# Performance work log

Measured on AMD Instinct MI355X. Metric: run time of the kernel, lower is better.

Reference implementation:

```python
import jax, jax.numpy as jnp
import numpy as np

B, S, D = 2, 2048, 1024
H, A = 16, 64  # num_heads, attention_dim


def setup_inputs() -> dict:
    key = jax.random.key(0)
    ks = jax.random.split(key, 9)
    sd = D ** -0.5
    so = (H * A) ** -0.5
    return {
        "x": jax.random.normal(ks[0], (B, S, D), dtype=jnp.float32),
        "Wq": jax.random.normal(ks[1], (D, H * A), dtype=jnp.float32) * sd,
        "bq": jnp.zeros((H * A,), dtype=jnp.float32),
        "Wk": jax.random.normal(ks[2], (D, H * A), dtype=jnp.float32) * sd,
        "bk": jnp.zeros((H * A,), dtype=jnp.float32),
        "Wv": jax.random.normal(ks[3], (D, H * A), dtype=jnp.float32) * sd,
        "bv": jnp.zeros((H * A,), dtype=jnp.float32),
        "Wo": jax.random.normal(ks[4], (H * A, D), dtype=jnp.float32) * so,
        "bo": jnp.zeros((D,), dtype=jnp.float32),
    }


def reference(x, Wq, bq, Wk, bk, Wv, bv, Wo, bo):
    b, s, _ = x.shape
    # project and split heads: [b, s, H, A]
    q = (x @ Wq + bq).reshape(b, s, H, A)
    k = (x @ Wk + bk).reshape(b, s, H, A)
    v = (x @ Wv + bv).reshape(b, s, H, A)
    # scores [b, H, s, s]
    scores = jnp.einsum("bqhd,bkhd->bhqk", q, k) / jnp.sqrt(jnp.float32(A))
    weights = jax.nn.softmax(scores, axis=-1)
    attended = jnp.einsum("bhqk,bkhd->bqhd", weights, v).reshape(b, s, H * A)
    return attended @ Wo + bo
```

## Files before the change

### kernel.cpp

```cpp
#include <hip/hip_runtime.h>
#include <hip/hip_bf16.h>

typedef __attribute__((ext_vector_type(8))) short bf16x8;
typedef __attribute__((ext_vector_type(4))) float f32x4;

#define LOG2E 1.44269504088896f

extern "C" __device__ float __ocml_native_exp2_f32(float);

__device__ __forceinline__ unsigned short f2bf(float f) {
    union { float f; unsigned int u; } v; v.f = f;
    unsigned int r = v.u + 0x7FFF + ((v.u >> 16) & 1);
    return (unsigned short)(r >> 16);
}

__device__ __forceinline__ unsigned int pk_bf16(float lo, float hi) {
    unsigned int r;
    asm("v_cvt_pk_bf16_f32 %0, %1, %2" : "=v"(r) : "v"(lo), "v"(hi));
    return r;
}

typedef __attribute__((address_space(3))) unsigned int lds_uint;
typedef __attribute__((address_space(1))) const unsigned int glob_uint;
__device__ __forceinline__ void gl2lds16(const void* g, void* l) {
    __builtin_amdgcn_global_load_lds((glob_uint*)g, (lds_uint*)l, 16, 0, 0);
}

__global__ __launch_bounds__(256) void cvt_bf16(const float* __restrict__ in,
                                                unsigned int* __restrict__ out, int n4) {
    int i = blockIdx.x * 256 + threadIdx.x;
    if (i >= n4) return;
    float4 v = ((const float4*)in)[i];
    uint2 o;
    o.x = pk_bf16(v.x, v.y);
    o.y = pk_bf16(v.z, v.w);
    ((uint2*)out)[i] = o;
}

__global__ __launch_bounds__(256) void transpose4_bf16(
    const float* __restrict__ w0, const float* __restrict__ w1,
    const float* __restrict__ w2, const float* __restrict__ w3,
    unsigned short* __restrict__ o0, unsigned short* __restrict__ o1,
    unsigned short* __restrict__ o2, unsigned short* __restrict__ o3) {
    const int z = blockIdx.z;
    const float* in = (z == 0) ? w0 : (z == 1) ? w1 : (z == 2) ? w2 : w3;
    unsigned short* out = (z == 0) ? o0 : (z == 1) ? o1 : (z == 2) ? o2 : o3;
    __shared__ float t[32][33];
    int tx = threadIdx.x & 31, ty = threadIdx.x >> 5;
    int r0 = blockIdx.y * 32, c0 = blockIdx.x * 32;
    for (int i = 0; i < 32; i += 8)
        t[ty + i][tx] = in[(size_t)(r0 + ty + i) * 1024 + c0 + tx];
    __syncthreads();
    for (int i = 0; i < 32; i += 8)
        out[(size_t)(c0 + ty + i) * 1024 + r0 + tx] = f2bf(t[tx][ty + i]);
}

__device__ __forceinline__ void gemm_core(const short* __restrict__ A,
                                          const short* __restrict__ BT,
                                          int K, int bm0, int bn0,
                                          short* sm, f32x4 acc[4][4]) {
    const int tid = threadIdx.x;
    const int lane = tid & 63;
    const int w = tid >> 6;
    const int wr0 = (w >> 1) * 64;
    const int wc0 = (w & 1) * 64;
    const int l15 = lane & 15, quad = lane >> 4;
    const int sr = lane >> 2;
    const int slog = (lane & 3) ^ (sr & 3) ^ (sr >> 2);

#pragma unroll
    for (int i = 0; i < 4; i++)
#pragma unroll
        for (int j = 0; j < 4; j++) acc[i][j] = (f32x4)0.f;

    const short* sp[4];
    int sdo[4];
#pragma unroll
    for (int i = 0; i < 4; i++) {
        int c = w * 4 + i;
        sp[i] = (c < 8) ? A + (size_t)(bm0 + c * 16 + sr) * K + slog * 8
                        : BT + (size_t)(bn0 + (c - 8) * 16 + sr) * K + slog * 8;
        sdo[i] = c * 512;
    }
    auto stage = [&](int buf) {
        short* bb = sm + buf * 8192;
#pragma unroll
        for (int i = 0; i < 4; i++) {
            gl2lds16(sp[i], bb + sdo[i]);
            sp[i] += 32;
        }
    };
    const int ph = (quad ^ (l15 & 3) ^ (l15 >> 2)) * 8;
    auto compute = [&](int buf) {
        const short* Ab = sm + buf * 8192;
        const short* Bb = Ab + 4096;
        bf16x8 af[4], bfr[4];
#pragma unroll
        for (int im = 0; im < 4; im++)
            af[im] = *(const bf16x8*)&Ab[(wr0 + im * 16 + l15) * 32 + ph];
#pragma unroll
        for (int in = 0; in < 4; in++)
            bfr[in] = *(const bf16x8*)&Bb[(wc0 + in * 16 + l15) * 32 + ph];
        __builtin_amdgcn_s_setprio(1);
#pragma unroll
        for (int im = 0; im < 4; im++)
#pragma unroll
            for (int in = 0; in < 4; in++)
                acc[im][in] = __builtin_amdgcn_mfma_f32_16x16x32_bf16(af[im], bfr[in], acc[im][in], 0, 0, 0);
        __builtin_amdgcn_s_setprio(0);
    };

    stage(0); stage(1);
    asm volatile("s_waitcnt vmcnt(4)" ::: "memory");
    __builtin_amdgcn_s_barrier();
    asm volatile("" ::: "memory");

    const int nt = K >> 5;
    int bs = 2, bc = 0;
    for (int t = 0; t < nt - 2; ++t) {
        stage(bs); bs = (bs == 2) ? 0 : bs + 1;
        compute(bc); bc = (bc == 2) ? 0 : bc + 1;
        asm volatile("s_waitcnt vmcnt(4)" ::: "memory");
        __builtin_amdgcn_s_barrier();
        asm volatile("" ::: "memory");
    }
    compute(bc); bc = (bc == 2) ? 0 : bc + 1;
    asm volatile("s_waitcnt vmcnt(0)" ::: "memory");
    __builtin_amdgcn_s_barrier();
    asm volatile("" ::: "memory");
    compute(bc);
}

__global__ __launch_bounds__(256) void gemm_qkv(
    const short* __restrict__ xb,
    const short* __restrict__ wqT, const short* __restrict__ wkT, const short* __restrict__ wvT,
    const float* __restrict__ bq, const float* __restrict__ bk, const float* __restrict__ bv,
    unsigned short* __restrict__ qb, unsigned short* __restrict__ kb, unsigned short* __restrict__ vTb) {
    __shared__ short sm[24576];
    const int z = blockIdx.z;
    const short* Amat = (z == 2) ? wvT : xb;
    const short* Bmat = (z == 0) ? wqT : (z == 1) ? wkT : xb;
    const float* bias = (z == 0) ? bq : (z == 1) ? bk : bv;
    const float scl = (z == 0) ? 0.125f * LOG2E : 1.f;
    const int bm0 = (z == 2) ? blockIdx.y * 128 : blockIdx.x * 128;
    const int bn0 = (z == 2) ? blockIdx.x * 128 : blockIdx.y * 128;
    f32x4 acc[4][4];
    gemm_core(Amat, Bmat, 1024, bm0, bn0, sm, acc);
    const int lane = threadIdx.x & 63, w = threadIdx.x >> 6;
    const int wr0 = (w >> 1) * 64, wc0 = (w & 1) * 64, l15 = lane & 15, quad = lane >> 4;
    if (z == 2) {
        for (int im = 0; im < 4; im++)
            for (int in = 0; in < 4; in++)
                for (int r = 0; r < 4; r++) {
                    int rowa = bm0 + wr0 + im * 16 + quad * 4 + r;
                    int colg = bn0 + wc0 + in * 16 + l15;
                    unsigned short ov = f2bf(acc[im][in][r] + bias[rowa]);
                    int b = colg >> 11, s = colg & 2047;
                    vTb[(size_t)b * 2097152 + (size_t)rowa * 2048 + s] = ov;
                }
    } else {
        for (int im = 0; im < 4; im++)
            for (int in = 0; in < 4; in++)
                for (int r = 0; r < 4; r++) {
                    int rowg = bm0 + wr0 + im * 16 + quad * 4 + r;
                    int colg = bn0 + wc0 + in * 16 + l15;
                    unsigned short ov = f2bf((acc[im][in][r] + bias[colg]) * scl);
                    int b = rowg >> 11, s = rowg & 2047;
                    int h = colg >> 6, a = colg & 63;
                    int bh = b * 16 + h;
                    if (z == 0) qb[((size_t)bh * 2048 + s) * 64 + a] = ov;
                    else        kb[((size_t)bh * 2048 + s) * 64 + a] = ov;
                }
    }
}

__global__ __launch_bounds__(256) void gemm_out(
    const short* __restrict__ att, const short* __restrict__ woT,
    const float* __restrict__ bo, float* __restrict__ out) {
    __shared__ short sm[24576];
    const int bm0 = blockIdx.x * 128, bn0 = blockIdx.y * 128;
    f32x4 acc[4][4];
    gemm_core(att, woT, 1024, bm0, bn0, sm, acc);
    const int lane = threadIdx.x & 63, w = threadIdx.x >> 6;
    const int wr0 = (w >> 1) * 64, wc0 = (w & 1) * 64, l15 = lane & 15, quad = lane >> 4;
    for (int im = 0; im < 4; im++)
        for (int in = 0; in < 4; in++)
            for (int r = 0; r < 4; r++) {
                int rowg = bm0 + wr0 + im * 16 + quad * 4 + r;
                int colg = bn0 + wc0 + in * 16 + l15;
                out[(size_t)rowg * 1024 + colg] = acc[im][in][r] + bo[colg];
            }
}

__global__ __launch_bounds__(512, 4) void flash_attn(
    const unsigned short* __restrict__ qb, const unsigned short* __restrict__ kb,
    const unsigned short* __restrict__ vTb, unsigned short* __restrict__ att) {
    __shared__ short Qs[8192];
    __shared__ short Ks[4][4096];
    __shared__ short Vs[4][4096];
    const int tid = threadIdx.x, lane = tid & 63, w = tid >> 6;
    const int l15 = lane & 15, quad = lane >> 4;
    const int q0 = blockIdx.x * 128;
    const int bh = blockIdx.y;
    const size_t qkbase = (size_t)bh * 2048 * 64;
    const size_t vbase = (size_t)bh * 64 * 2048;
    const int sr = lane >> 3;
    const int slog = (lane & 7) ^ sr;
    const int l7 = l15 & 7;

    const unsigned short* sgp;
    int sgstep, sg2;
    short* sgb;
    if (w < 4) {
        sgp = kb + qkbase + (size_t)(w * 16 + sr) * 64 + slog * 8;
        sgstep = 4096; sg2 = 512;
        sgb = &Ks[0][0] + w * 1024;
    } else {
        sgp = vTb + vbase + (size_t)((w - 4) * 16 + sr) * 2048 + slog * 8;
        sgstep = 64; sg2 = 16384;
        sgb = &Vs[0][0] + (w - 4) * 1024;
    }
    auto stage_tile = [&](int buf) {
        short* sd = sgb + buf * 4096;
        gl2lds16(sgp, sd);
        gl2lds16(sgp + sg2, sd + 512);
        sgp += sgstep;
    };

    for (int i = 0; i < 2; i++) {
        int c = w * 2 + i;
        gl2lds16(qb + qkbase + (size_t)(q0 + c * 8 + sr) * 64 + slog * 8, Qs + c * 512);
    }
    stage_tile(0); stage_tile(1); stage_tile(2);
    asm volatile("s_waitcnt vmcnt(4)" ::: "memory");
    __builtin_amdgcn_s_barrier();
    asm volatile("" ::: "memory");

    const int wq0 = w * 16;
    const int c0 = (quad ^ l7) * 8, c1 = c0 ^ 32;
    const int fb = l15 * 64;
    bf16x8 aq0 = *(const bf16x8*)&Qs[(wq0 + l15) * 64 + c0];
    bf16x8 aq1 = *(const bf16x8*)&Qs[(wq0 + l15) * 64 + c1];

    f32x4 o[4];
    for (int dt = 0; dt < 4; dt++) o[dt] = (f32x4)0.f;
    f32x4 ls = (f32x4)0.f;

    auto attn_step = [&](int buf) {
        const short* Kb = &Ks[0][0] + buf * 4096;
        const short* Vb = &Vs[0][0] + buf * 4096;
        f32x4 sc[4];
        __builtin_amdgcn_s_setprio(1);
#pragma unroll
        for (int t = 0; t < 4; t++) {
            bf16x8 ak = *(const bf16x8*)(Kb + fb + c0 + t * 1024);
            sc[t] = __builtin_amdgcn_mfma_f32_16x16x32_bf16(ak, aq0, (f32x4)0.f, 0, 0, 0);
        }
#pragma unroll
        for (int t = 0; t < 4; t++) {
            bf16x8 ak = *(const bf16x8*)(Kb + fb + c1 + t * 1024);
            sc[t] = __builtin_amdgcn_mfma_f32_16x16x32_bf16(ak, aq1, sc[t], 0, 0, 0);
        }
        __builtin_amdgcn_s_setprio(0);
#pragma unroll
        for (int t = 0; t < 4; t++) {
#pragma unroll
            for (int r = 0; r < 4; r++) sc[t][r] = __ocml_native_exp2_f32(sc[t][r]);
            ls += sc[t];
        }
        bf16x8 bp[2];
#pragma unroll
        for (int t2 = 0; t2 < 2; t2++) {
            unsigned pa = pk_bf16(sc[2 * t2][0], sc[2 * t2][1]);
            unsigned pb = pk_bf16(sc[2 * t2][2], sc[2 * t2][3]);
            unsigned pc = pk_bf16(sc[2 * t2 + 1][0], sc[2 * t2 + 1][1]);
            unsigned pd = pk_bf16(sc[2 * t2 + 1][2], sc[2 * t2 + 1][3]);
            asm("v_permlane32_swap_b32 %0, %1" : "+v"(pa), "+v"(pc));
            asm("v_permlane32_swap_b32 %0, %1" : "+v"(pb), "+v"(pd));
            asm("v_permlane16_swap_b32 %0, %1" : "+v"(pa), "+v"(pc));
            asm("v_permlane16_swap_b32 %0, %1" : "+v"(pb), "+v"(pd));
            union { unsigned u[4]; bf16x8 v; } cvt;
            cvt.u[0] = pa; cvt.u[1] = pb; cvt.u[2] = pc; cvt.u[3] = pd;
            bp[t2] = cvt.v;
        }
        __builtin_amdgcn_s_setprio(1);
#pragma unroll
        for (int t2 = 0; t2 < 2; t2++) {
            const int cc = t2 ? c1 : c0;
#pragma unroll
            for (int dt = 0; dt < 4; dt++) {
                bf16x8 av = *(const bf16x8*)(Vb + fb + cc + dt * 1024);
                o[dt] = __builtin_amdgcn_mfma_f32_16x16x32_bf16(av, bp[t2], o[dt], 0, 0, 0);
            }
        }
        __builtin_amdgcn_s_setprio(0);
    };

    for (int t = 0; t < 29; t++) {
        stage_tile((t + 3) & 3);
        attn_step(t & 3);
        asm volatile("s_waitcnt vmcnt(4)" ::: "memory");
        __builtin_amdgcn_s_barrier();
        asm volatile("" ::: "memory");
    }
    attn_step(1);
    asm volatile("s_waitcnt vmcnt(2)" ::: "memory");
    __builtin_amdgcn_s_barrier();
    asm volatile("" ::: "memory");
    attn_step(2);
    asm volatile("s_waitcnt vmcnt(0)" ::: "memory");
    __builtin_amdgcn_s_barrier();
    asm volatile("" ::: "memory");
    attn_step(3);

    const int b = bh >> 4, h = bh & 15;
    float l = (ls[0] + ls[1]) + (ls[2] + ls[3]);
    l += __shfl_xor(l, 16);
    l += __shfl_xor(l, 32);
    float inv = 1.f / l;
    int s = q0 + wq0 + l15;
    for (int dt = 0; dt < 4; dt++) {
        uint2 pk;
        pk.x = pk_bf16(o[dt][0] * inv, o[dt][1] * inv);
        pk.y = pk_bf16(o[dt][2] * inv, o[dt][3] * inv);
        int col = h * 64 + dt * 16 + quad * 4;
        *(uint2*)&att[((size_t)b * 2048 + s) * 1024 + col] = pk;
    }
}

extern "C" void kernel_launch(void* const* d_in, const int* in_sizes, int n_in,
                              void* d_out, int out_size, void* d_ws, size_t ws_size,
                              hipStream_t stream) {
    const float* x  = (const float*)d_in[0];
    const float* Wq = (const float*)d_in[1];
    const float* bq = (const float*)d_in[2];
    const float* Wk = (const float*)d_in[3];
    const float* bk = (const float*)d_in[4];
    const float* Wv = (const float*)d_in[5];
    const float* bv = (const float*)d_in[6];
    const float* Wo = (const float*)d_in[7];
    const float* bo = (const float*)d_in[8];
    float* out = (float*)d_out;

    short* ws  = (short*)d_ws;
    short* xb  = ws;
    short* wqT = ws + 4 * 1024 * 1024;
    short* wkT = wqT + 1024 * 1024;
    short* wvT = wkT + 1024 * 1024;
    short* woT = wvT + 1024 * 1024;
    short* qb  = woT + 1024 * 1024;
    short* kb  = qb + 4 * 1024 * 1024;
    short* vTb = kb + 4 * 1024 * 1024;
    short* att = vTb + 4 * 1024 * 1024;

    cvt_bf16<<<4096, 256, 0, stream>>>(x, (unsigned int*)xb, 1024 * 1024);
    transpose4_bf16<<<dim3(32, 32, 4), 256, 0, stream>>>(
        Wq, Wk, Wv, Wo,
        (unsigned short*)wqT, (unsigned short*)wkT,
        (unsigned short*)wvT, (unsigned short*)woT);
    gemm_qkv<<<dim3(32, 8, 3), 256, 0, stream>>>(xb, wqT, wkT, wvT, bq, bk, bv,
                                                 (unsigned short*)qb, (unsigned short*)kb,
                                                 (unsigned short*)vTb);
    flash_attn<<<dim3(16, 32), 512, 0, stream>>>((const unsigned short*)qb,
                                                 (const unsigned short*)kb,
                                                 (const unsigned short*)vTb,
                                                 (unsigned short*)att);
    gemm_out<<<dim3(32, 8), 256, 0, stream>>>(att, woT, bo, out);
}
```

Baseline: 182.3 us.

## Halve flash-attention block to 4 waves, each wave processing 32 query rows

The flash attention kernel now runs 256 threads per block instead of 512. Each wave handles two 16-row query tiles and reuses every K and V fragment it loads from LDS for both tiles, which halves LDS reads per MFMA. Each wave also stages twice as many K/V chunks per tile, so the vmcnt waits are doubled to match. In exchange there is more register pressure from the doubled accumulators, fewer waves per block to hide latency, and an occupancy hint lowered to 2.

```diff
diff --git a/kernel.cpp b/kernel.cpp
--- a/kernel.cpp
+++ b/kernel.cpp
@@ -192,7 +192,7 @@
             }
 }
 
-__global__ __launch_bounds__(512, 4) void flash_attn(
+__global__ __launch_bounds__(256, 2) void flash_attn(
     const unsigned short* __restrict__ qb, const unsigned short* __restrict__ kb,
     const unsigned short* __restrict__ vTb, unsigned short* __restrict__ att) {
     __shared__ short Qs[8192];
@@ -209,66 +209,58 @@
     const int l7 = l15 & 7;
 
     const unsigned short* sgp;
-    int sgstep, sg2;
+    int sgstep, sgr;
     short* sgb;
-    if (w < 4) {
-        sgp = kb + qkbase + (size_t)(w * 16 + sr) * 64 + slog * 8;
-        sgstep = 4096; sg2 = 512;
-        sgb = &Ks[0][0] + w * 1024;
+    if (w < 2) {
+        sgp = kb + qkbase + (size_t)(w * 32 + sr) * 64 + slog * 8;
+        sgstep = 4096;
+        sgr = 512;
+        sgb = &Ks[0][0] + w * 2048;
     } else {
-        sgp = vTb + vbase + (size_t)((w - 4) * 16 + sr) * 2048 + slog * 8;
-        sgstep = 64; sg2 = 16384;
-        sgb = &Vs[0][0] + (w - 4) * 1024;
+        sgp = vTb + vbase + (size_t)((w - 2) * 32 + sr) * 2048 + slog * 8;
+        sgstep = 64;
+        sgr = 16384;
+        sgb = &Vs[0][0] + (w - 2) * 2048;
     }
     auto stage_tile = [&](int buf) {
         short* sd = sgb + buf * 4096;
         gl2lds16(sgp, sd);
-        gl2lds16(sgp + sg2, sd + 512);
+        gl2lds16(sgp + sgr, sd + 512);
+        gl2lds16(sgp + 2 * sgr, sd + 1024);
+        gl2lds16(sgp + 3 * sgr, sd + 1536);
         sgp += sgstep;
     };
 
-    for (int i = 0; i < 2; i++) {
-        int c = w * 2 + i;
+#pragma unroll
+    for (int i = 0; i < 4; i++) {
+        int c = w * 4 + i;
         gl2lds16(qb + qkbase + (size_t)(q0 + c * 8 + sr) * 64 + slog * 8, Qs + c * 512);
     }
     stage_tile(0); stage_tile(1); stage_tile(2);
-    asm volatile("s_waitcnt vmcnt(4)" ::: "memory");
-    __builtin_amdgcn_s_barrier();
-    asm volatile("" ::: "memory");
-
-    const int wq0 = w * 16;
+    asm volatile("s_waitcnt vmcnt(8)" ::: "memory");
+    __builtin_amdgcn_s_barrier();
+    asm volatile("" ::: "memory");
+
+    const int wq0 = w * 32;
     const int c0 = (quad ^ l7) * 8, c1 = c0 ^ 32;
     const int fb = l15 * 64;
-    bf16x8 aq0 = *(const bf16x8*)&Qs[(wq0 + l15) * 64 + c0];
-    bf16x8 aq1 = *(const bf16x8*)&Qs[(wq0 + l15) * 64 + c1];
-
-    f32x4 o[4];
-    for (int dt = 0; dt < 4; dt++) o[dt] = (f32x4)0.f;
-    f32x4 ls = (f32x4)0.f;
-
-    auto attn_step = [&](int buf) {
-        const short* Kb = &Ks[0][0] + buf * 4096;
-        const short* Vb = &Vs[0][0] + buf * 4096;
-        f32x4 sc[4];
-        __builtin_amdgcn_s_setprio(1);
+    bf16x8 aq00 = *(const bf16x8*)&Qs[(wq0 + l15) * 64 + c0];
+    bf16x8 aq01 = *(const bf16x8*)&Qs[(wq0 + l15) * 64 + c1];
+    bf16x8 aq10 = *(const bf16x8*)&Qs[(wq0 + 16 + l15) * 64 + c0];
+    bf16x8 aq11 = *(const bf16x8*)&Qs[(wq0 + 16 + l15) * 64 + c1];
+
+    f32x4 o0[4], o1[4];
+#pragma unroll
+    for (int dt = 0; dt < 4; dt++) { o0[dt] = (f32x4)0.f; o1[dt] = (f32x4)0.f; }
+    f32x4 ls0 = (f32x4)0.f, ls1 = (f32x4)0.f;
+
+    auto smax = [&](f32x4 (&sc)[4], f32x4& lsr, bf16x8 (&bp)[2]) {
 #pragma unroll
         for (int t = 0; t < 4; t++) {
-            bf16x8 ak = *(const bf16x8*)(Kb + fb + c0 + t * 1024);
-            sc[t] = __builtin_amdgcn_mfma_f32_16x16x32_bf16(ak, aq0, (f32x4)0.f, 0, 0, 0);
-        }
-#pragma unroll
-        for (int t = 0; t < 4; t++) {
-            bf16x8 ak = *(const bf16x8*)(Kb + fb + c1 + t * 1024);
-            sc[t] = __builtin_amdgcn_mfma_f32_16x16x32_bf16(ak, aq1, sc[t], 0, 0, 0);
-        }
-        __builtin_amdgcn_s_setprio(0);
-#pragma unroll
-        for (int t = 0; t < 4; t++) {
 #pragma unroll
             for (int r = 0; r < 4; r++) sc[t][r] = __ocml_native_exp2_f32(sc[t][r]);
-            ls += sc[t];
-        }
-        bf16x8 bp[2];
+            lsr += sc[t];
+        }
 #pragma unroll
         for (int t2 = 0; t2 < 2; t2++) {
             unsigned pa = pk_bf16(sc[2 * t2][0], sc[2 * t2][1]);
@@ -283,6 +275,29 @@
             cvt.u[0] = pa; cvt.u[1] = pb; cvt.u[2] = pc; cvt.u[3] = pd;
             bp[t2] = cvt.v;
         }
+    };
+
+    auto attn_step = [&](int buf) {
+        const short* Kb = &Ks[0][0] + buf * 4096;
+        const short* Vb = &Vs[0][0] + buf * 4096;
+        f32x4 sc0[4], sc1[4];
+        __builtin_amdgcn_s_setprio(1);
+#pragma unroll
+        for (int t = 0; t < 4; t++) {
+            bf16x8 ak = *(const bf16x8*)(Kb + fb + c0 + t * 1024);
+            sc0[t] = __builtin_amdgcn_mfma_f32_16x16x32_bf16(ak, aq00, (f32x4)0.f, 0, 0, 0);
+            sc1[t] = __builtin_amdgcn_mfma_f32_16x16x32_bf16(ak, aq10, (f32x4)0.f, 0, 0, 0);
+        }
+#pragma unroll
+        for (int t = 0; t < 4; t++) {
+            bf16x8 ak = *(const bf16x8*)(Kb + fb + c1 + t * 1024);
+            sc0[t] = __builtin_amdgcn_mfma_f32_16x16x32_bf16(ak, aq01, sc0[t], 0, 0, 0);
+            sc1[t] = __builtin_amdgcn_mfma_f32_16x16x32_bf16(ak, aq11, sc1[t], 0, 0, 0);
+        }
+        __builtin_amdgcn_s_setprio(0);
+        bf16x8 bp0[2], bp1[2];
+        smax(sc0, ls0, bp0);
+        smax(sc1, ls1, bp1);
         __builtin_amdgcn_s_setprio(1);
 #pragma unroll
         for (int t2 = 0; t2 < 2; t2++) {
@@ -290,7 +305,8 @@
 #pragma unroll
             for (int dt = 0; dt < 4; dt++) {
                 bf16x8 av = *(const bf16x8*)(Vb + fb + cc + dt * 1024);
-                o[dt] = __builtin_amdgcn_mfma_f32_16x16x32_bf16(av, bp[t2], o[dt], 0, 0, 0);
+                o0[dt] = __builtin_amdgcn_mfma_f32_16x16x32_bf16(av, bp0[t2], o0[dt], 0, 0, 0);
+                o1[dt] = __builtin_amdgcn_mfma_f32_16x16x32_bf16(av, bp1[t2], o1[dt], 0, 0, 0);
             }
         }
         __builtin_amdgcn_s_setprio(0);
@@ -299,12 +315,12 @@
     for (int t = 0; t < 29; t++) {
         stage_tile((t + 3) & 3);
         attn_step(t & 3);
-        asm volatile("s_waitcnt vmcnt(4)" ::: "memory");
+        asm volatile("s_waitcnt vmcnt(8)" ::: "memory");
         __builtin_amdgcn_s_barrier();
         asm volatile("" ::: "memory");
     }
     attn_step(1);
-    asm volatile("s_waitcnt vmcnt(2)" ::: "memory");
+    asm volatile("s_waitcnt vmcnt(4)" ::: "memory");
     __builtin_amdgcn_s_barrier();
     asm volatile("" ::: "memory");
     attn_step(2);
@@ -314,17 +330,25 @@
     attn_step(3);
 
     const int b = bh >> 4, h = bh & 15;
-    float l = (ls[0] + ls[1]) + (ls[2] + ls[3]);
-    l += __shfl_xor(l, 16);
-    l += __shfl_xor(l, 32);
-    float inv = 1.f / l;
+    float l0 = (ls0[0] + ls0[1]) + (ls0[2] + ls0[3]);
+    l0 += __shfl_xor(l0, 16);
+    l0 += __shfl_xor(l0, 32);
+    float inv0 = 1.f / l0;
+    float l1 = (ls1[0] + ls1[1]) + (ls1[2] + ls1[3]);
+    l1 += __shfl_xor(l1, 16);
+    l1 += __shfl_xor(l1, 32);
+    float inv1 = 1.f / l1;
     int s = q0 + wq0 + l15;
+#pragma unroll
     for (int dt = 0; dt < 4; dt++) {
+        int col = h * 64 + dt * 16 + quad * 4;
         uint2 pk;
-        pk.x = pk_bf16(o[dt][0] * inv, o[dt][1] * inv);
-        pk.y = pk_bf16(o[dt][2] * inv, o[dt][3] * inv);
-        int col = h * 64 + dt * 16 + quad * 4;
+        pk.x = pk_bf16(o0[dt][0] * inv0, o0[dt][1] * inv0);
+        pk.y = pk_bf16(o0[dt][2] * inv0, o0[dt][3] * inv0);
         *(uint2*)&att[((size_t)b * 2048 + s) * 1024 + col] = pk;
+        pk.x = pk_bf16(o1[dt][0] * inv1, o1[dt][1] * inv1);
+        pk.y = pk_bf16(o1[dt][2] * inv1, o1[dt][3] * inv1);
+        *(uint2*)&att[((size_t)b * 2048 + s + 16) * 1024 + col] = pk;
     }
 }
 
@@ -361,7 +385,7 @@
     gemm_qkv<<<dim3(32, 8, 3), 256, 0, stream>>>(xb, wqT, wkT, wvT, bq, bk, bv,
                                                  (unsigned short*)qb, (unsigned short*)kb,
                                                  (unsigned short*)vTb);
-    flash_attn<<<dim3(16, 32), 512, 0, stream>>>((const unsigned short*)qb,
+    flash_attn<<<dim3(16, 32), 256, 0, stream>>>((const unsigned short*)qb,
                                                  (const unsigned short*)kb,
                                                  (const unsigned short*)vTb,
                                                  (unsigned short*)att);
```

Result: no change. 185.5 us (+1.8%).
